# Optimization experiments

Hardware: AMD Instinct MI355X
Metric: run time of the kernel (lower is better)

## Reference

```python
import jax, jax.numpy as jnp
import numpy as np

B, S, D = 4, 2048, 1024
NEG = -1e9

def setup_inputs() -> dict:
    key = jax.random.key(0)
    ks = jax.random.split(key, 12)
    sc = 1.0 / np.sqrt(D)
    inp = {
        'query': jax.random.normal(ks[0], (B, S, D), jnp.float32),
        'key':   jax.random.normal(ks[1], (B, S, D), jnp.float32),
        'value': jax.random.normal(ks[2], (B, S, D), jnp.float32),
        'Wq': jax.random.normal(ks[3], (D, D), jnp.float32) * sc,
        'bq': jnp.zeros((D,), jnp.float32),
        'Wk': jax.random.normal(ks[4], (D, D), jnp.float32) * sc,
        'bk': jnp.zeros((D,), jnp.float32),
        'Wv': jax.random.normal(ks[5], (D, D), jnp.float32) * sc,
        'bv': jnp.zeros((D,), jnp.float32),
        'Wo': jax.random.normal(ks[6], (D, D), jnp.float32) * sc,
        'bo': jnp.zeros((D,), jnp.float32),
    }
    return inp

def reference(query, key, value, Wq, bq, Wk, bk, Wv, bv, Wo, bo):
    d_model = query.shape[-1]
    q = query @ Wq + bq            # [B,S,D]
    k = key   @ Wk + bk
    v = value @ Wv + bv
    # scores scaled by sqrt(d_model) (single head, full d_model)
    scores = jnp.einsum('bqd,bkd->bqk', q, k) / jnp.sqrt(jnp.float32(d_model))
    s = scores.shape[-1]
    causal = jnp.tril(jnp.ones((s, s), bool))  # True = keep
    scores = jnp.where(causal, scores, NEG)
    # log-softmax then exp for numerical stability (use_log_probs=True)
    attn = jnp.exp(jax.nn.log_softmax(scores, axis=-1))
    out = jnp.einsum('bqk,bkd->bqd', attn, v)
    return out @ Wo + bo
```

## Files before the change

kernel.cpp:

```cpp
#include <hip/hip_runtime.h>


typedef __attribute__((ext_vector_type(8))) short bf16x8_t;
typedef __attribute__((ext_vector_type(4))) float f32x4_t;

static __device__ __forceinline__ unsigned short f2b(float f) {
  union { float f; unsigned u; } c; c.f = f;
  unsigned u = c.u;
  u += 0x7fffu + ((u >> 16) & 1u);
  return (unsigned short)(u >> 16);
}

static __device__ __forceinline__ void gload16(const void* g, const void* l) {
  __builtin_amdgcn_global_load_lds(
      (const __attribute__((address_space(1))) void*)g,
      (__attribute__((address_space(3))) void*)(void*)(unsigned short*)l,
      16, 0, 0);
}

__global__ __launch_bounds__(256)
void cast3_bf16(const float* __restrict__ q, const float* __restrict__ k,
                const float* __restrict__ v,
                unsigned short* __restrict__ oq, unsigned short* __restrict__ ok,
                unsigned short* __restrict__ ov)
{
  const int z = blockIdx.z;
  const float* in = z == 0 ? q : (z == 1 ? k : v);
  unsigned short* out = z == 0 ? oq : (z == 1 ? ok : ov);
  const size_t base = ((size_t)blockIdx.x * 256 + threadIdx.x) * 8;
  const float4 x0 = *(const float4*)(in + base);
  const float4 x1 = *(const float4*)(in + base + 4);
  union { unsigned u[4]; uint4 v4; } pk;
  pk.u[0] = f2b(x0.x) | ((unsigned)f2b(x0.y) << 16);
  pk.u[1] = f2b(x0.z) | ((unsigned)f2b(x0.w) << 16);
  pk.u[2] = f2b(x1.x) | ((unsigned)f2b(x1.y) << 16);
  pk.u[3] = f2b(x1.z) | ((unsigned)f2b(x1.w) << 16);
  *(uint4*)(out + base) = pk.v4;
}

template<bool HAS_BIAS, bool OUT_BF16>
static __device__ __forceinline__
void gemm_body(const unsigned short* __restrict__ Ab,
               const unsigned short* __restrict__ Bt,
               const float* __restrict__ bias, void* __restrict__ Cp,
               int kEnd, int lda, int ldb, int ldc, float scale, int bx, int by)
{
  __shared__ unsigned short As[128 * 64];
  __shared__ unsigned short Bs[128 * 64];

  const int tid  = threadIdx.x;
  const int lane = tid & 63;
  const int wid  = tid >> 6;
  const int wr   = wid >> 1, wc = wid & 1;
  const int l15  = lane & 15, l4 = lane >> 4;

  const int srow_l = lane >> 3;
  const int schk   = lane & 7;

  f32x4_t acc[4][4];
#pragma unroll
  for (int m = 0; m < 4; ++m)
#pragma unroll
    for (int n = 0; n < 4; ++n) acc[m][n] = (f32x4_t){0.f, 0.f, 0.f, 0.f};

  for (int k0 = 0; k0 < kEnd; k0 += 64) {
#pragma unroll
    for (int i = 0; i < 4; ++i) {
      const int row = i * 32 + wid * 8 + srow_l;
      const size_t gr = (size_t)(by * 128 + row);
      const int g = schk ^ (row & 7);
      gload16(Ab + gr * lda + k0 + g * 8, &As[(i * 32 + wid * 8) * 64]);
    }
#pragma unroll
    for (int i = 0; i < 4; ++i) {
      const int row = i * 32 + wid * 8 + srow_l;
      const size_t gn = (size_t)(bx * 128 + row);
      const int g = schk ^ (row & 7);
      gload16(Bt + gn * ldb + k0 + g * 8, &Bs[(i * 32 + wid * 8) * 64]);
    }
    __syncthreads();

#pragma unroll
    for (int kk = 0; kk < 2; ++kk) {
      bf16x8_t a[4], b[4];
#pragma unroll
      for (int m = 0; m < 4; ++m) {
        const int row = wr * 64 + m * 16 + l15;
        const int c = (kk * 4 + l4) ^ (row & 7);
        a[m] = *(const bf16x8_t*)&As[row * 64 + c * 8];
      }
#pragma unroll
      for (int n = 0; n < 4; ++n) {
        const int row = wc * 64 + n * 16 + l15;
        const int c = (kk * 4 + l4) ^ (row & 7);
        b[n] = *(const bf16x8_t*)&Bs[row * 64 + c * 8];
      }
#pragma unroll
      for (int m = 0; m < 4; ++m)
#pragma unroll
        for (int n = 0; n < 4; ++n)
          acc[m][n] = __builtin_amdgcn_mfma_f32_16x16x32_bf16(a[m], b[n], acc[m][n], 0, 0, 0);
    }
    __syncthreads();
  }

  float*          Cf = (float*)Cp;
  unsigned short* Cb = (unsigned short*)Cp;
#pragma unroll
  for (int m = 0; m < 4; ++m)
#pragma unroll
    for (int n = 0; n < 4; ++n) {
      const int col = bx * 128 + wc * 64 + n * 16 + l15;
      const float bv = HAS_BIAS ? bias[col] : 0.f;
#pragma unroll
      for (int j = 0; j < 4; ++j) {
        const int row = by * 128 + wr * 64 + m * 16 + l4 * 4 + j;
        const float val = acc[m][n][j] * scale + bv;
        if (OUT_BF16) Cb[(size_t)row * ldc + col] = f2b(val);
        else          Cf[(size_t)row * ldc + col] = val;
      }
    }
}

__global__ __launch_bounds__(256)
void gemm_qkv(const unsigned short* __restrict__ qi,
              const unsigned short* __restrict__ ki,
              const unsigned short* __restrict__ vi,
              const unsigned short* __restrict__ Wq,
              const unsigned short* __restrict__ Wk,
              const unsigned short* __restrict__ Wv,
              const float* __restrict__ bq, const float* __restrict__ bk,
              const float* __restrict__ bv,
              unsigned short* __restrict__ oq, unsigned short* __restrict__ ok,
              unsigned short* __restrict__ ov)
{
  const int d = blockIdx.x;
  const int xcd = d & 7, j = d >> 3;
  const int G = xcd * 24 + (j >> 3);
  const int z = G >> 6;
  const int by = G & 63;
  const int bx = j & 7;
  const unsigned short* A = z == 0 ? qi : (z == 1 ? ki : vi);
  const unsigned short* B = z == 0 ? Wq : (z == 1 ? Wk : Wv);
  const float* bias = z == 0 ? bq : (z == 1 ? bk : bv);
  unsigned short* C = z == 0 ? oq : (z == 1 ? ok : ov);
  gemm_body<true, true>(A, B, bias, C, 1024, 1024, 1024, 1024, 1.f, bx, by);
}

__global__ __launch_bounds__(256)
void gemm_scores(const unsigned short* __restrict__ Q,
                 const unsigned short* __restrict__ Kb, float* __restrict__ S)
{
  const int d = blockIdx.x;
  const int t = (d & 7) * 68 + (d >> 3);
  const int bz = t / 136;
  const int tri = t - bz * 136;
  int by = (int)((sqrtf(8.f * tri + 1.f) - 1.f) * 0.5f);
  while ((by + 1) * (by + 2) / 2 <= tri) ++by;
  while (by * (by + 1) / 2 > tri) --by;
  const int bx = tri - by * (by + 1) / 2;
  gemm_body<false, false>(Q + (size_t)bz * 2048 * 1024,
                          Kb + (size_t)bz * 2048 * 1024, nullptr,
                          S + (size_t)bz * 2048 * 2048,
                          1024, 1024, 1024, 2048, 0.03125f, bx, by);
}

__global__ __launch_bounds__(256)
void gemm_pv(const unsigned short* __restrict__ P,
             const unsigned short* __restrict__ Vt, unsigned short* __restrict__ C)
{
  const int d = blockIdx.x;
  const int xcd = d & 7, j = d >> 3;
  const int G = xcd * 8 + (j >> 3);
  const int bz = G >> 4;
  const int by = G & 15;
  const int bx = j & 7;
  const int kEnd = (by + 1) * 128;
  gemm_body<false, true>(P + (size_t)bz * 2048 * 4096,
                         Vt + (size_t)bz * 1024 * 2048, nullptr,
                         C + (size_t)bz * 2048 * 1024,
                         kEnd, 4096, 2048, 1024, 1.f, bx, by);
}

__global__ __launch_bounds__(256)
void gemm_out(const unsigned short* __restrict__ ctx,
              const unsigned short* __restrict__ Wo,
              const float* __restrict__ bo, float* __restrict__ out)
{
  const int d = blockIdx.x;
  const int xcd = d & 7, j = d >> 3;
  const int by = xcd * 8 + (j >> 3);
  const int bx = j & 7;
  gemm_body<true, false>(ctx, Wo, bo, out, 1024, 1024, 1024, 1024, 1.f, bx, by);
}

__global__ __launch_bounds__(256)
void transpose4_w(const float* __restrict__ w0, const float* __restrict__ w1,
                  const float* __restrict__ w2, const float* __restrict__ w3,
                  unsigned short* __restrict__ o0, unsigned short* __restrict__ o1,
                  unsigned short* __restrict__ o2, unsigned short* __restrict__ o3)
{
  __shared__ unsigned short t[32][34];
  const int z = blockIdx.z;
  const float* in = z == 0 ? w0 : (z == 1 ? w1 : (z == 2 ? w2 : w3));
  unsigned short* out = z == 0 ? o0 : (z == 1 ? o1 : (z == 2 ? o2 : o3));
  const int bx = blockIdx.x, by = blockIdx.y;
  const int x = threadIdx.x, y = threadIdx.y;
#pragma unroll
  for (int yy = y; yy < 32; yy += 8)
    t[yy][x] = f2b(in[(size_t)(by * 32 + yy) * 1024 + bx * 32 + x]);
  __syncthreads();
#pragma unroll
  for (int yy = y; yy < 32; yy += 8)
    out[(size_t)(bx * 32 + yy) * 1024 + by * 32 + x] = t[x][yy];
}

__global__ __launch_bounds__(256)
void transpose_v(const unsigned short* __restrict__ in, unsigned short* __restrict__ out)
{
  __shared__ unsigned short t[32][34];
  const int bx = blockIdx.x;
  const int by = blockIdx.y;
  const int bz = blockIdx.z;
  const int x = threadIdx.x, y = threadIdx.y;
  const unsigned short* inb = in + (size_t)bz * 2048 * 1024;
  unsigned short* ob = out + (size_t)bz * 1024 * 2048;
#pragma unroll
  for (int yy = y; yy < 32; yy += 8)
    t[yy][x] = inb[(size_t)(by * 32 + yy) * 1024 + bx * 32 + x];
  __syncthreads();
#pragma unroll
  for (int yy = y; yy < 32; yy += 8)
    ob[(size_t)(bx * 32 + yy) * 2048 + by * 32 + x] = t[x][yy];
}

__global__ __launch_bounds__(256)
void softmax_rows(const float* __restrict__ S, unsigned short* __restrict__ P)
{
  const int row = blockIdx.x;
  const int q = row & 2047;
  const float* srow = S + (size_t)row * 2048;
  unsigned short* prow = P + (size_t)row * 4096;
  const int nvalid = q + 1;
  const int kend = ((q >> 7) + 1) << 7;
  const int tid = threadIdx.x;
  const int wid = tid >> 6, lane = tid & 63;
  const int base = tid * 8;

  const float4 x0 = *(const float4*)(srow + base);
  const float4 x1 = *(const float4*)(srow + base + 4);
  float v[8] = {x0.x, x0.y, x0.z, x0.w, x1.x, x1.y, x1.z, x1.w};

  float m = -1e30f;
#pragma unroll
  for (int i = 0; i < 8; ++i) {
    if (base + i >= nvalid) v[i] = -1e30f;
    m = fmaxf(m, v[i]);
  }
#pragma unroll
  for (int off = 32; off > 0; off >>= 1) m = fmaxf(m, __shfl_xor(m, off));
  __shared__ float redm[4];
  __shared__ float reds[4];
  if (lane == 0) redm[wid] = m;
  __syncthreads();
  m = fmaxf(fmaxf(redm[0], redm[1]), fmaxf(redm[2], redm[3]));

  float s = 0.f;
  float e[8];
#pragma unroll
  for (int i = 0; i < 8; ++i) {
    e[i] = (base + i < nvalid) ? __expf(v[i] - m) : 0.f;
    s += e[i];
  }
#pragma unroll
  for (int off = 32; off > 0; off >>= 1) s += __shfl_xor(s, off);
  if (lane == 0) reds[wid] = s;
  __syncthreads();
  s = reds[0] + reds[1] + reds[2] + reds[3];
  const float inv = 1.f / s;

  if (base < kend) {
    union { unsigned u[4]; uint4 v4; } pk;
#pragma unroll
    for (int i = 0; i < 4; ++i) {
      const unsigned lo = f2b(e[2 * i] * inv);
      const unsigned hi = f2b(e[2 * i + 1] * inv);
      pk.u[i] = lo | (hi << 16);
    }
    *(uint4*)(prow + base) = pk.v4;
  }
}

extern "C" void kernel_launch(void* const* d_in, const int* in_sizes, int n_in,
                              void* d_out, int out_size, void* d_ws, size_t ws_size,
                              hipStream_t stream)
{
  const float* query = (const float*)d_in[0];
  const float* key   = (const float*)d_in[1];
  const float* value = (const float*)d_in[2];
  const float* Wq    = (const float*)d_in[3];
  const float* bq    = (const float*)d_in[4];
  const float* Wk    = (const float*)d_in[5];
  const float* bk    = (const float*)d_in[6];
  const float* Wv    = (const float*)d_in[7];
  const float* bv    = (const float*)d_in[8];
  const float* Wo    = (const float*)d_in[9];
  const float* bo    = (const float*)d_in[10];
  float* out = (float*)d_out;

  char* ws = (char*)d_ws;
  const size_t MB = 1024 * 1024;
  unsigned short* Wqt  = (unsigned short*)(ws + 0 * MB);
  unsigned short* Wkt  = (unsigned short*)(ws + 2 * MB);
  unsigned short* Wvt  = (unsigned short*)(ws + 4 * MB);
  unsigned short* Wot  = (unsigned short*)(ws + 6 * MB);
  unsigned short* qbuf = (unsigned short*)(ws + 8 * MB);
  unsigned short* kbuf = (unsigned short*)(ws + 24 * MB);
  unsigned short* vbuf = (unsigned short*)(ws + 40 * MB);
  unsigned short* vT   = (unsigned short*)(ws + 56 * MB);
  float*          Sraw = (float*)(ws + 72 * MB);
  unsigned short* qin  = (unsigned short*)(ws + 72 * MB);
  unsigned short* kin  = (unsigned short*)(ws + 88 * MB);
  unsigned short* vin  = (unsigned short*)(ws + 104 * MB);
  unsigned short* ctx  = (unsigned short*)(ws + 136 * MB);

  cast3_bf16<<<dim3(4096, 1, 3), 256, 0, stream>>>(query, key, value, qin, kin, vin);

  transpose4_w<<<dim3(32, 32, 4), dim3(32, 8), 0, stream>>>(
      Wq, Wk, Wv, Wo, Wqt, Wkt, Wvt, Wot);

  gemm_qkv<<<1536, 256, 0, stream>>>(
      qin, kin, vin, Wqt, Wkt, Wvt, bq, bk, bv, qbuf, kbuf, vbuf);

  transpose_v<<<dim3(32, 64, 4), dim3(32, 8), 0, stream>>>(vbuf, vT);

  gemm_scores<<<544, 256, 0, stream>>>(qbuf, kbuf, Sraw);

  softmax_rows<<<8192, 256, 0, stream>>>(Sraw, (unsigned short*)Sraw);

  gemm_pv<<<512, 256, 0, stream>>>((unsigned short*)Sraw, vT, ctx);

  gemm_out<<<512, 256, 0, stream>>>(ctx, Wot, bo, out);
}
```

Measured before the change: 347.2 us.

## Fold output projection into value projection via precomputed Wv·Wo

```diff
diff --git a/kernel.cpp b/kernel.cpp
--- a/kernel.cpp
+++ b/kernel.cpp
@@ -16,6 +16,17 @@
       (const __attribute__((address_space(1))) void*)g,
       (__attribute__((address_space(3))) void*)(void*)(unsigned short*)l,
       16, 0, 0);
+}
+
+__global__ __launch_bounds__(256)
+void bias2_k(const float* __restrict__ bv, const float* __restrict__ Wo,
+             const float* __restrict__ bo, float* __restrict__ bias2)
+{
+  const int d = blockIdx.x * 256 + threadIdx.x;
+  float s = bo[d];
+#pragma unroll 8
+  for (int j = 0; j < 1024; ++j) s += bv[j] * Wo[(size_t)j * 1024 + d];
+  bias2[d] = s;
 }
 
 __global__ __launch_bounds__(256)
@@ -38,7 +49,36 @@
   *(uint4*)(out + base) = pk.v4;
 }
 
-template<bool HAS_BIAS, bool OUT_BF16>
+__global__ __launch_bounds__(256)
+void prep_w(const float* __restrict__ wq, const float* __restrict__ wk,
+            const float* __restrict__ wo, const float* __restrict__ wv,
+            unsigned short* __restrict__ oq, unsigned short* __restrict__ ok,
+            unsigned short* __restrict__ oo, unsigned short* __restrict__ ov)
+{
+  __shared__ unsigned short t[32][34];
+  const int z = blockIdx.z;
+  const float* in = z == 0 ? wq : (z == 1 ? wk : (z == 2 ? wo : wv));
+  unsigned short* out = z == 0 ? oq : (z == 1 ? ok : (z == 2 ? oo : ov));
+  const int bx = blockIdx.x, by = blockIdx.y;
+  const int x = threadIdx.x, y = threadIdx.y;
+  if (z == 3) {
+#pragma unroll
+    for (int yy = y; yy < 32; yy += 8) {
+      const int r = by * 32 + yy, c = bx * 32 + x;
+      out[(size_t)r * 1024 + c] = f2b(in[(size_t)r * 1024 + c]);
+    }
+    return;
+  }
+#pragma unroll
+  for (int yy = y; yy < 32; yy += 8)
+    t[yy][x] = f2b(in[(size_t)(by * 32 + yy) * 1024 + bx * 32 + x]);
+  __syncthreads();
+#pragma unroll
+  for (int yy = y; yy < 32; yy += 8)
+    out[(size_t)(bx * 32 + yy) * 1024 + by * 32 + x] = t[x][yy];
+}
+
+template<bool OUT_BF16>
 static __device__ __forceinline__
 void gemm_body(const unsigned short* __restrict__ Ab,
                const unsigned short* __restrict__ Bt,
@@ -111,7 +151,7 @@
 #pragma unroll
     for (int n = 0; n < 4; ++n) {
       const int col = bx * 128 + wc * 64 + n * 16 + l15;
-      const float bv = HAS_BIAS ? bias[col] : 0.f;
+      const float bv = bias ? bias[col] : 0.f;
 #pragma unroll
       for (int j = 0; j < 4; ++j) {
         const int row = by * 128 + wr * 64 + m * 16 + l4 * 4 + j;
@@ -123,16 +163,24 @@
 }
 
 __global__ __launch_bounds__(256)
+void gemm_wvo(const unsigned short* __restrict__ Wot,
+              const unsigned short* __restrict__ Wvb,
+              unsigned short* __restrict__ WvoT)
+{
+  gemm_body<true>(Wot, Wvb, nullptr, WvoT, 1024, 1024, 1024, 1024, 1.f,
+                  blockIdx.x & 7, blockIdx.x >> 3);
+}
+
+__global__ __launch_bounds__(256)
 void gemm_qkv(const unsigned short* __restrict__ qi,
               const unsigned short* __restrict__ ki,
               const unsigned short* __restrict__ vi,
               const unsigned short* __restrict__ Wq,
               const unsigned short* __restrict__ Wk,
-              const unsigned short* __restrict__ Wv,
+              const unsigned short* __restrict__ WvoT,
               const float* __restrict__ bq, const float* __restrict__ bk,
-              const float* __restrict__ bv,
               unsigned short* __restrict__ oq, unsigned short* __restrict__ ok,
-              unsigned short* __restrict__ ov)
+              unsigned short* __restrict__ ovwo)
 {
   const int d = blockIdx.x;
   const int xcd = d & 7, j = d >> 3;
@@ -141,10 +189,10 @@
   const int by = G & 63;
   const int bx = j & 7;
   const unsigned short* A = z == 0 ? qi : (z == 1 ? ki : vi);
-  const unsigned short* B = z == 0 ? Wq : (z == 1 ? Wk : Wv);
-  const float* bias = z == 0 ? bq : (z == 1 ? bk : bv);
-  unsigned short* C = z == 0 ? oq : (z == 1 ? ok : ov);
-  gemm_body<true, true>(A, B, bias, C, 1024, 1024, 1024, 1024, 1.f, bx, by);
+  const unsigned short* B = z == 0 ? Wq : (z == 1 ? Wk : WvoT);
+  const float* bias = z == 0 ? bq : (z == 1 ? bk : nullptr);
+  unsigned short* C = z == 0 ? oq : (z == 1 ? ok : ovwo);
+  gemm_body<true>(A, B, bias, C, 1024, 1024, 1024, 1024, 1.f, bx, by);
 }
 
 __global__ __launch_bounds__(256)
@@ -159,15 +207,16 @@
   while ((by + 1) * (by + 2) / 2 <= tri) ++by;
   while (by * (by + 1) / 2 > tri) --by;
   const int bx = tri - by * (by + 1) / 2;
-  gemm_body<false, false>(Q + (size_t)bz * 2048 * 1024,
-                          Kb + (size_t)bz * 2048 * 1024, nullptr,
-                          S + (size_t)bz * 2048 * 2048,
-                          1024, 1024, 1024, 2048, 0.03125f, bx, by);
-}
-
-__global__ __launch_bounds__(256)
-void gemm_pv(const unsigned short* __restrict__ P,
-             const unsigned short* __restrict__ Vt, unsigned short* __restrict__ C)
+  gemm_body<false>(Q + (size_t)bz * 2048 * 1024,
+                   Kb + (size_t)bz * 2048 * 1024, nullptr,
+                   S + (size_t)bz * 2048 * 2048,
+                   1024, 1024, 1024, 2048, 0.03125f, bx, by);
+}
+
+__global__ __launch_bounds__(256)
+void gemm_final(const unsigned short* __restrict__ P,
+                const unsigned short* __restrict__ VwoT,
+                const float* __restrict__ bias2, float* __restrict__ out)
 {
   const int d = blockIdx.x;
   const int xcd = d & 7, j = d >> 3;
@@ -176,43 +225,10 @@
   const int by = G & 15;
   const int bx = j & 7;
   const int kEnd = (by + 1) * 128;
-  gemm_body<false, true>(P + (size_t)bz * 2048 * 4096,
-                         Vt + (size_t)bz * 1024 * 2048, nullptr,
-                         C + (size_t)bz * 2048 * 1024,
-                         kEnd, 4096, 2048, 1024, 1.f, bx, by);
-}
-
-__global__ __launch_bounds__(256)
-void gemm_out(const unsigned short* __restrict__ ctx,
-              const unsigned short* __restrict__ Wo,
-              const float* __restrict__ bo, float* __restrict__ out)
-{
-  const int d = blockIdx.x;
-  const int xcd = d & 7, j = d >> 3;
-  const int by = xcd * 8 + (j >> 3);
-  const int bx = j & 7;
-  gemm_body<true, false>(ctx, Wo, bo, out, 1024, 1024, 1024, 1024, 1.f, bx, by);
-}
-
-__global__ __launch_bounds__(256)
-void transpose4_w(const float* __restrict__ w0, const float* __restrict__ w1,
-                  const float* __restrict__ w2, const float* __restrict__ w3,
-                  unsigned short* __restrict__ o0, unsigned short* __restrict__ o1,
-                  unsigned short* __restrict__ o2, unsigned short* __restrict__ o3)
-{
-  __shared__ unsigned short t[32][34];
-  const int z = blockIdx.z;
-  const float* in = z == 0 ? w0 : (z == 1 ? w1 : (z == 2 ? w2 : w3));
-  unsigned short* out = z == 0 ? o0 : (z == 1 ? o1 : (z == 2 ? o2 : o3));
-  const int bx = blockIdx.x, by = blockIdx.y;
-  const int x = threadIdx.x, y = threadIdx.y;
-#pragma unroll
-  for (int yy = y; yy < 32; yy += 8)
-    t[yy][x] = f2b(in[(size_t)(by * 32 + yy) * 1024 + bx * 32 + x]);
-  __syncthreads();
-#pragma unroll
-  for (int yy = y; yy < 32; yy += 8)
-    out[(size_t)(bx * 32 + yy) * 1024 + by * 32 + x] = t[x][yy];
+  gemm_body<false>(P + (size_t)bz * 2048 * 4096,
+                   VwoT + (size_t)bz * 1024 * 2048, bias2,
+                   out + (size_t)bz * 2048 * 1024,
+                   kEnd, 4096, 2048, 1024, 1.f, bx, by);
 }
 
 __global__ __launch_bounds__(256)
@@ -310,35 +326,38 @@
 
   char* ws = (char*)d_ws;
   const size_t MB = 1024 * 1024;
-  unsigned short* Wqt  = (unsigned short*)(ws + 0 * MB);
-  unsigned short* Wkt  = (unsigned short*)(ws + 2 * MB);
-  unsigned short* Wvt  = (unsigned short*)(ws + 4 * MB);
-  unsigned short* Wot  = (unsigned short*)(ws + 6 * MB);
-  unsigned short* qbuf = (unsigned short*)(ws + 8 * MB);
-  unsigned short* kbuf = (unsigned short*)(ws + 24 * MB);
-  unsigned short* vbuf = (unsigned short*)(ws + 40 * MB);
-  unsigned short* vT   = (unsigned short*)(ws + 56 * MB);
-  float*          Sraw = (float*)(ws + 72 * MB);
-  unsigned short* qin  = (unsigned short*)(ws + 72 * MB);
-  unsigned short* kin  = (unsigned short*)(ws + 88 * MB);
-  unsigned short* vin  = (unsigned short*)(ws + 104 * MB);
-  unsigned short* ctx  = (unsigned short*)(ws + 136 * MB);
+  unsigned short* Wqt   = (unsigned short*)(ws + 0 * MB);
+  unsigned short* Wkt   = (unsigned short*)(ws + 2 * MB);
+  unsigned short* Wot   = (unsigned short*)(ws + 4 * MB);
+  unsigned short* Wvb   = (unsigned short*)(ws + 6 * MB);
+  unsigned short* WvoT  = (unsigned short*)(ws + 8 * MB);
+  float*          bias2 = (float*)(ws + 10 * MB);
+  unsigned short* qbuf  = (unsigned short*)(ws + 12 * MB);
+  unsigned short* kbuf  = (unsigned short*)(ws + 28 * MB);
+  unsigned short* vwo   = (unsigned short*)(ws + 44 * MB);
+  unsigned short* vwoT  = (unsigned short*)(ws + 60 * MB);
+  float*          Sraw  = (float*)(ws + 80 * MB);
+  unsigned short* qin   = (unsigned short*)(ws + 80 * MB);
+  unsigned short* kin   = (unsigned short*)(ws + 96 * MB);
+  unsigned short* vin   = (unsigned short*)(ws + 112 * MB);
+
+  bias2_k<<<4, 256, 0, stream>>>(bv, Wo, bo, bias2);
 
   cast3_bf16<<<dim3(4096, 1, 3), 256, 0, stream>>>(query, key, value, qin, kin, vin);
 
-  transpose4_w<<<dim3(32, 32, 4), dim3(32, 8), 0, stream>>>(
-      Wq, Wk, Wv, Wo, Wqt, Wkt, Wvt, Wot);
+  prep_w<<<dim3(32, 32, 4), dim3(32, 8), 0, stream>>>(
+      Wq, Wk, Wo, Wv, Wqt, Wkt, Wot, Wvb);
+
+  gemm_wvo<<<64, 256, 0, stream>>>(Wot, Wvb, WvoT);
 
   gemm_qkv<<<1536, 256, 0, stream>>>(
-      qin, kin, vin, Wqt, Wkt, Wvt, bq, bk, bv, qbuf, kbuf, vbuf);
-
-  transpose_v<<<dim3(32, 64, 4), dim3(32, 8), 0, stream>>>(vbuf, vT);
+      qin, kin, vin, Wqt, Wkt, WvoT, bq, bk, qbuf, kbuf, vwo);
+
+  transpose_v<<<dim3(32, 64, 4), dim3(32, 8), 0, stream>>>(vwo, vwoT);
 
   gemm_scores<<<544, 256, 0, stream>>>(qbuf, kbuf, Sraw);
 
   softmax_rows<<<8192, 256, 0, stream>>>(Sraw, (unsigned short*)Sraw);
 
-  gemm_pv<<<512, 256, 0, stream>>>((unsigned short*)Sraw, vT, ctx);
-
-  gemm_out<<<512, 256, 0, stream>>>(ctx, Wot, bo, out);
-}
+  gemm_final<<<512, 256, 0, stream>>>((unsigned short*)Sraw, vwoT, bias2, out);
+}
```

Result: slower. 418.9 us (+20.6%).
